# Kernel optimization log

Measured on AMD Instinct MI355X. Metric: run time of the kernel, lower is better.

The kernel has to match this reference:

```python
import jax, jax.numpy as jnp
import numpy as np

H = W = 256          # full-res feature map (2h x 2w)
WIN = 16             # window size
STRIDE = 2           # shifted-window stride
HEADS = 8
DIM_HEAD = 64
INNER = HEADS * DIM_HEAD
DIM = 128
KEEP = 50            # min(int(0.7*(256//16)**2), 50)
IOU_THR = 0.2


def _make_windows():
    xs = np.arange(0, W - WIN + 1, STRIDE)
    ys = np.arange(0, H - WIN + 1, STRIDE)
    gx, gy = np.meshgrid(xs, ys)
    return np.stack([gx.ravel(), gy.ravel(), gx.ravel() + WIN - 1, gy.ravel() + WIN - 1], axis=1)

_WIN_NP = _make_windows()          # [M,4] = (x1,y1,x2,y2), M = 121*121 = 14641
BOXES = jnp.asarray(_WIN_NP, dtype=jnp.float32)
SXY = jnp.asarray(_WIN_NP[:, :2], dtype=jnp.int32)   # integer (sx, sy) origins

# torchvision roi_align (spatial_scale=1, sampling_ratio->ceil(15/16)=1, aligned=False):
_off = (np.arange(WIN) + 0.5) * (WIN - 1.0) / WIN
LO = jnp.asarray(np.floor(_off).astype(np.int32))      # low integer index, in [0,14]
FR = jnp.asarray((_off - np.floor(_off)).astype(np.float32))


def _nms_keep(scores):
    """Greedy NMS over the fixed window grid; returns top-KEEP kept indices."""
    x1, y1, x2, y2 = BOXES[:, 0], BOXES[:, 1], BOXES[:, 2], BOXES[:, 3]
    area = (x2 - x1) * (y2 - y1)

    def body(k, carry):
        live, keep = carry
        idx = jnp.argmax(jnp.where(live, scores, -jnp.inf))
        bb = BOXES[idx]
        iw = jnp.clip(jnp.minimum(x2, bb[2]) - jnp.maximum(x1, bb[0]), 0.0)
        ih = jnp.clip(jnp.minimum(y2, bb[3]) - jnp.maximum(y1, bb[1]), 0.0)
        inter = iw * ih
        iou = inter / (area + area[idx] - inter)
        live = live & (iou <= IOU_THR)
        return live, keep.at[k].set(idx.astype(jnp.int32))

    _, keep = jax.lax.fori_loop(
        0, KEEP, body,
        (jnp.ones(BOXES.shape[0], bool), jnp.zeros(KEEP, jnp.int32)))
    return keep


def _forward(x, prob, fix_w, w_qkv, w_out, b_out):
    b = prob.shape[0]
    d = x.shape[-1]
    # entropy map at half res
    entropy = -jnp.sum(prob * jnp.log2(prob + 1e-10), axis=1)          # [b,128,128]
    # FixCNN: 8x8 ones-init conv, VALID -> [b,1,121,121]; normalized window score
    score = jax.lax.conv_general_dilated(
        entropy[:, None], fix_w, (1, 1), 'VALID',
        dimension_numbers=('NCHW', 'OIHW', 'NCHW'))
    score = score.reshape(b, -1) / float((WIN // 2) * (WIN // 2))      # [b,14641]

    keep = jax.lax.stop_gradient(jax.vmap(_nms_keep)(score))           # [b,KEEP]
    sx = SXY[keep][..., 0]                                             # [b,KEEP]
    sy = SXY[keep][..., 1]

    x2d = x.reshape(b, H, W, d)   # token n = h*W + w (channels-last layout)
    ar = jnp.arange(WIN)

    def gather_one(xi, syi, sxi):  # xi [H,W,d]
        R = syi[:, None, None] + ar[None, :, None]
        C = sxi[:, None, None] + ar[None, None, :]
        return xi[R, C]

    crops = jax.vmap(gather_one)(x2d, sy, sx)                          # [b,K,16,16,d]

    # roi_align bilinear sampling with fixed fractional grid
    c00 = crops[:, :, LO[:, None], LO[None, :]]
    c01 = crops[:, :, LO[:, None], LO[None, :] + 1]
    c10 = crops[:, :, LO[:, None] + 1, LO[None, :]]
    c11 = crops[:, :, LO[:, None] + 1, LO[None, :] + 1]
    fy = FR[:, None, None]
    fx = FR[None, :, None]
    win = ((1 - fy) * (1 - fx) * c00 + (1 - fy) * fx * c01
           + fy * (1 - fx) * c10 + fy * fx * c11)                      # [b,K,16,16,d]

    toks = win.reshape(b * KEEP, WIN * WIN, d)                         # [m,256,d]
    qkv = toks @ w_qkv.T                                               # [m,256,3*INNER]
    q, k_, v = jnp.split(qkv, 3, axis=-1)

    def to_heads(t):
        return t.reshape(t.shape[0], t.shape[1], HEADS, DIM_HEAD).transpose(0, 2, 1, 3)

    q, k_, v = to_heads(q), to_heads(k_), to_heads(v)
    attn = jax.nn.softmax(jnp.einsum('mhnd,mhkd->mhnk', q, k_) * (DIM_HEAD ** -0.5), axis=-1)
    out = jnp.einsum('mhnk,mhkd->mhnd', attn, v)
    out = out.transpose(0, 2, 1, 3).reshape(b * KEEP, WIN * WIN, INNER)
    out = out @ w_out.T + b_out                                        # [m,256,d]

    # overlap scatter-add + count normalization
    out2d = out.reshape(b, KEEP, WIN, WIN, d)
    bidx = jnp.arange(b)[:, None, None, None]
    Y = sy[:, :, None, None] + ar[None, None, :, None]
    X = sx[:, :, None, None] + ar[None, None, None, :]
    acc = jnp.zeros((b, H, W, d), x.dtype).at[bidx, Y, X].add(out2d)
    cnt = jnp.zeros((b, H, W), x.dtype).at[bidx, Y, X].add(1.0)
    outx = (acc / (cnt[..., None] + 1e-10)).reshape(b, H * W, d)
    return x + outx


def setup_inputs() -> dict:
    key = jax.random.key(0)
    ks = jax.random.split(key, 4)
    b = 4
    x = jax.random.normal(ks[0], (b, H * W, DIM), dtype=jnp.float32)
    prob = jax.random.uniform(ks[1], (b, 2, H // 2, W // 2), dtype=jnp.float32)
    fix_w = jnp.ones((1, 1, WIN // 2, WIN // 2), dtype=jnp.float32)
    w_qkv = jax.random.normal(ks[2], (3 * INNER, DIM), dtype=jnp.float32) * 0.02
    w_out = jax.random.normal(ks[3], (DIM, INNER), dtype=jnp.float32) * 0.02
    b_out = jnp.zeros((DIM,), dtype=jnp.float32)
    return {"x": x, "prob": prob, "fix_w": fix_w, "w_qkv": w_qkv, "w_out": w_out, "b_out": b_out}


def reference(x, prob, fix_w, w_qkv, w_out, b_out):
    return _forward(x, prob, fix_w, w_qkv, w_out, b_out)
```

## Files before the change

kernel.cpp:

```cpp
#include <hip/hip_runtime.h>
#include <math.h>

#define NB 4
#define NWIN 121
#define NBOX (NWIN*NWIN)
#define NKEEP 50
#define HWD 256
#define DIM 128
#define HEADS 8
#define NTOK 256
#define NWTOT (NB*NKEEP)

#define OFF_ENT   0
#define OFF_SCORE 65536
#define OFF_KEEP  124160
#define OFF_WQKV  124288
#define OFF_WOUT  222592
#define OFF_TOKBF 255360
#define OFF_PO    3532160
#define WS_FLOATS 6808960

#define KPAD 76
#define VPAD 268

typedef __attribute__((ext_vector_type(8))) short short8;
typedef __attribute__((ext_vector_type(4))) short short4v;
typedef __attribute__((ext_vector_type(4))) float f32x4;

static __device__ __forceinline__ unsigned short f2bf(float f) {
  union { float f; unsigned u; } v; v.f = f;
  unsigned r = (v.u + 0x7fffu + ((v.u >> 16) & 1u)) >> 16;
  return (unsigned short)r;
}
static __device__ __forceinline__ short4v pk4(f32x4 a) {
  short4v r;
  r[0] = (short)f2bf(a[0]); r[1] = (short)f2bf(a[1]);
  r[2] = (short)f2bf(a[2]); r[3] = (short)f2bf(a[3]);
  return r;
}
static __device__ __forceinline__ short8 ld8_lds(const unsigned short* p) {
  short4v a = *(const short4v*)p;
  short4v b = *(const short4v*)(p + 4);
  short8 r;
  r[0]=a[0]; r[1]=a[1]; r[2]=a[2]; r[3]=a[3];
  r[4]=b[0]; r[5]=b[1]; r[6]=b[2]; r[7]=b[3];
  return r;
}
static __device__ __forceinline__ short8 ld8_g(const unsigned short* p) {
  return *(const short8*)p;
}

template<int CTRL>
static __device__ __forceinline__ float dppmax(float v) {
  union { float f; int i; } a, r; a.f = v;
  r.i = __builtin_amdgcn_update_dpp(a.i, a.i, CTRL, 0xf, 0xf, false);
  return fmaxf(v, r.f);
}

__global__ void k_entropy(const float* __restrict__ prob, float* __restrict__ ent) {
  int idx = blockIdx.x * 256 + threadIdx.x;
  int b = idx >> 14, p = idx & 16383;
  float p0 = prob[(size_t)(b * 2) * 16384 + p];
  float p1 = prob[(size_t)(b * 2 + 1) * 16384 + p];
  ent[idx] = -(p0 * log2f(p0 + 1e-10f) + p1 * log2f(p1 + 1e-10f));
}

__global__ void k_score(const float* __restrict__ ent, const float* __restrict__ fw,
                        float* __restrict__ sc) {
  int gid = blockIdx.x * 256 + threadIdx.x;
  if (gid >= NB * NBOX) return;
  int b = gid / NBOX, rem = gid % NBOX;
  int oy = rem / NWIN, ox = rem % NWIN;
  const float* e = ent + b * 16384 + oy * 128 + ox;
  float s = 0.f;
#pragma unroll
  for (int r = 0; r < 8; ++r)
#pragma unroll
    for (int c = 0; c < 8; ++c)
      s += e[r * 128 + c] * fw[r * 8 + c];
  sc[gid] = s * (1.0f / 64.0f);
}

__global__ void k_nms(const float* __restrict__ scores, int* __restrict__ keep) {
  __shared__ float sc[NWIN * 128];
  int b = blockIdx.x, l = threadIdx.x;
  for (int idx = l; idx < NWIN * 128; idx += 64) {
    int r = idx >> 7, c = idx & 127;
    float v = (c < NWIN) ? scores[b * NBOX + r * NWIN + c] : -INFINITY;
    sc[(r << 7) + (c ^ ((r & 7) << 2))] = v;
  }
  float M0 = -INFINITY, M1 = -INFINITY; int C0 = 0, C1 = 0;
#pragma unroll
  for (int slot = 0; slot < 2; ++slot) {
    int r = l + slot * 64;
    if (slot == 1 && r >= NWIN) break;
    int r7 = (r & 7) << 2, rbase = r << 7;
    float bv0=-INFINITY,bv1=-INFINITY,bv2=-INFINITY,bv3=-INFINITY;
    int bc0=0,bc1=0,bc2=0,bc3=0;
    for (int lb = 0; lb < 32; ++lb) {
      f32x4 v = *(const f32x4*)&sc[rbase + ((lb << 2) ^ r7)];
      int c0 = lb << 2;
      if (v[0] > bv0) { bv0 = v[0]; bc0 = c0; }
      if (v[1] > bv1) { bv1 = v[1]; bc1 = c0 + 1; }
      if (v[2] > bv2) { bv2 = v[2]; bc2 = c0 + 2; }
      if (v[3] > bv3) { bv3 = v[3]; bc3 = c0 + 3; }
    }
    float bv = bv0; int bc = bc0;
    if (bv1 > bv || (bv1 == bv && bc1 < bc)) { bv = bv1; bc = bc1; }
    if (bv2 > bv || (bv2 == bv && bc2 < bc)) { bv = bv2; bc = bc2; }
    if (bv3 > bv || (bv3 == bv && bc3 < bc)) { bv = bv3; bc = bc3; }
    if (slot == 0) { M0 = bv; C0 = bc; } else { M1 = bv; C1 = bc; }
  }

  for (int k = 0; k < NKEEP; ++k) {
    float g = fmaxf(M0, M1);
    g = dppmax<0x111>(g); g = dppmax<0x112>(g);
    g = dppmax<0x114>(g); g = dppmax<0x118>(g);
    g = dppmax<0x142>(g); g = dppmax<0x143>(g);
    union { float f; int i; } gi, gm; gi.f = g;
    gm.i = __builtin_amdgcn_readlane(gi.i, 63);
    float gmax = gm.f;
    unsigned long long b0 = __ballot(M0 == gmax);
    unsigned long long b1 = __ballot(M1 == gmax);
    int R;
    if (b0) R = __ffsll((unsigned long long)b0) - 1;
    else    R = 64 + __ffsll((unsigned long long)b1) - 1;
    int Cc = (R < 64) ? __builtin_amdgcn_readlane(C0, R)
                      : __builtin_amdgcn_readlane(C1, R - 64);
    if (l == 0) {
      keep[(b * NKEEP + k) * 2 + 0] = 2 * R;
      keep[(b * NKEEP + k) * 2 + 1] = 2 * Cc;
    }
    bool kill0 = false, kill1 = false;
    {
      int dy = l - R, ady = dy < 0 ? -dy : dy;
      if (ady <= 4) {
        int ih = 15 - 2 * ady;
#pragma unroll
        for (int dx = -4; dx <= 4; ++dx) {
          int adx = dx < 0 ? -dx : dx;
          if ((15 - 2 * adx) * ih > 75) {
            int cc = Cc + dx;
            if ((unsigned)cc < (unsigned)NWIN)
              sc[(l << 7) + (cc ^ ((l & 7) << 2))] = -INFINITY;
          }
        }
        int adx = C0 - Cc; adx = adx < 0 ? -adx : adx;
        kill0 = (adx <= 4) && ((15 - 2 * adx) * ih > 75);
      }
    }
    if (l + 64 < NWIN) {
      int r1 = l + 64;
      int dy = r1 - R, ady = dy < 0 ? -dy : dy;
      if (ady <= 4) {
        int ih = 15 - 2 * ady;
#pragma unroll
        for (int dx = -4; dx <= 4; ++dx) {
          int adx = dx < 0 ? -dx : dx;
          if ((15 - 2 * adx) * ih > 75) {
            int cc = Cc + dx;
            if ((unsigned)cc < (unsigned)NWIN)
              sc[(r1 << 7) + (cc ^ ((r1 & 7) << 2))] = -INFINITY;
          }
        }
        int adx = C1 - Cc; adx = adx < 0 ? -adx : adx;
        kill1 = (adx <= 4) && ((15 - 2 * adx) * ih > 75);
      }
    }
    if (__any(kill0 | kill1)) {
      int r = kill0 ? l : (kill1 ? l + 64 : l);
      int r7 = (r & 7) << 2, rbase = r << 7;
      float bv0=-INFINITY,bv1=-INFINITY,bv2=-INFINITY,bv3=-INFINITY;
      int bc0=0,bc1=0,bc2=0,bc3=0;
      for (int lb = 0; lb < 32; ++lb) {
        f32x4 v = *(const f32x4*)&sc[rbase + ((lb << 2) ^ r7)];
        int c0 = lb << 2;
        if (v[0] > bv0) { bv0 = v[0]; bc0 = c0; }
        if (v[1] > bv1) { bv1 = v[1]; bc1 = c0 + 1; }
        if (v[2] > bv2) { bv2 = v[2]; bc2 = c0 + 2; }
        if (v[3] > bv3) { bv3 = v[3]; bc3 = c0 + 3; }
      }
      float bv = bv0; int bc = bc0;
      if (bv1 > bv || (bv1 == bv && bc1 < bc)) { bv = bv1; bc = bc1; }
      if (bv2 > bv || (bv2 == bv && bc2 < bc)) { bv = bv2; bc = bc2; }
      if (bv3 > bv || (bv3 == bv && bc3 < bc)) { bv = bv3; bc = bc3; }
      if (kill0) { M0 = bv; C0 = bc; }
      else if (kill1) { M1 = bv; C1 = bc; }
    }
  }
}

__global__ void k_wcvt(const float* __restrict__ wqkv, const float* __restrict__ wout,
                       unsigned short* __restrict__ wqkv_bf, unsigned short* __restrict__ wout_bf) {
  int i = blockIdx.x * 256 + threadIdx.x;
  if (i < 196608) wqkv_bf[i] = f2bf(wqkv[i]);
  int j = i - 196608;
  if (j >= 0 && j < 65536) wout_bf[j] = f2bf(wout[j]);
}

__global__ void k_toks(const float* __restrict__ x, const int* __restrict__ keep,
                       unsigned short* __restrict__ tokbf) {
  int w = blockIdx.x;
  int b = w / NKEEP;
  int sy = keep[w * 2 + 0], sx = keep[w * 2 + 1];
  int tid = threadIdx.x;
  int ch = tid & 127, th = tid >> 7;
  const float* xb = x + (size_t)b * 65536 * DIM;
  for (int it = 0; it < 128; ++it) {
    int tk = it * 2 + th;
    int i = tk >> 4, j = tk & 15;
    float offy = (i + 0.5f) * 0.9375f;
    float offx = (j + 0.5f) * 0.9375f;
    int li = (int)offy, lj = (int)offx;
    float fy = offy - (float)li, fx = offx - (float)lj;
    const float* p = xb + ((size_t)((sy + li) * HWD + (sx + lj))) * DIM + ch;
    float v00 = p[0], v01 = p[DIM], v10 = p[HWD * DIM], v11 = p[HWD * DIM + DIM];
    float w00 = (1.f - fy) * (1.f - fx), w01 = (1.f - fy) * fx;
    float w10 = fy * (1.f - fx), w11 = fy * fx;
    tokbf[((size_t)w * NTOK + tk) * DIM + ch] = f2bf(w00 * v00 + w01 * v01 + w10 * v10 + w11 * v11);
  }
}

__global__ __launch_bounds__(512, 2) void k_attn(
    const unsigned short* __restrict__ tokbf,
    const unsigned short* __restrict__ wqkv,
    const unsigned short* __restrict__ wout,
    unsigned short* __restrict__ po) {
  __shared__ __align__(16) char smem[112128];
  unsigned short* Klds = (unsigned short*)smem;
  unsigned short* VT   = (unsigned short*)(smem + 38912);
  const int tid = threadIdx.x;
  const int wv = tid >> 6, ln = tid & 63;
  const int lo = ln & 15, hi = ln >> 4;
  const int win = blockIdx.x;
  unsigned short* QP = (unsigned short*)(smem + 73216 + wv * 4864);
  const unsigned short* tw = tokbf + (size_t)win * NTOK * DIM;
  const int qrow = wv * 32;

  f32x4 pacc[8][2];
#pragma unroll
  for (int mf = 0; mf < 8; ++mf)
#pragma unroll
    for (int nf = 0; nf < 2; ++nf) pacc[mf][nf] = (f32x4){0.f,0.f,0.f,0.f};

  for (int h = 0; h < HEADS; ++h) {
    if (h) __syncthreads();

    {
      f32x4 kacc[4][2];
#pragma unroll
      for (int mf = 0; mf < 4; ++mf)
#pragma unroll
        for (int nf = 0; nf < 2; ++nf) kacc[mf][nf] = (f32x4){0.f,0.f,0.f,0.f};
#pragma unroll
      for (int kf = 0; kf < 4; ++kf) {
        short8 aw[4], bt[2];
#pragma unroll
        for (int mf = 0; mf < 4; ++mf)
          aw[mf] = ld8_g(wqkv + (size_t)(512 + h * 64 + mf * 16 + lo) * 128 + kf * 32 + hi * 8);
#pragma unroll
        for (int nf = 0; nf < 2; ++nf)
          bt[nf] = ld8_g(&tw[(qrow + nf * 16 + lo) * 128 + kf * 32 + hi * 8]);
#pragma unroll
        for (int mf = 0; mf < 4; ++mf)
#pragma unroll
          for (int nf = 0; nf < 2; ++nf)
            kacc[mf][nf] = __builtin_amdgcn_mfma_f32_16x16x32_bf16(aw[mf], bt[nf], kacc[mf][nf], 0, 0, 0);
      }
#pragma unroll
      for (int mf = 0; mf < 4; ++mf)
#pragma unroll
        for (int nf = 0; nf < 2; ++nf)
          *(short4v*)&Klds[(qrow + nf * 16 + lo) * KPAD + mf * 16 + hi * 4] = pk4(kacc[mf][nf]);
    }
    {
      f32x4 vacc[2][4];
#pragma unroll
      for (int mf = 0; mf < 2; ++mf)
#pragma unroll
        for (int nf = 0; nf < 4; ++nf) vacc[mf][nf] = (f32x4){0.f,0.f,0.f,0.f};
#pragma unroll
      for (int kf = 0; kf < 4; ++kf) {
        short8 at[2], bw[4];
#pragma unroll
        for (int mf = 0; mf < 2; ++mf)
          at[mf] = ld8_g(&tw[(qrow + mf * 16 + lo) * 128 + kf * 32 + hi * 8]);
#pragma unroll
        for (int nf = 0; nf < 4; ++nf)
          bw[nf] = ld8_g(wqkv + (size_t)(1024 + h * 64 + nf * 16 + lo) * 128 + kf * 32 + hi * 8);
#pragma unroll
        for (int mf = 0; mf < 2; ++mf)
#pragma unroll
          for (int nf = 0; nf < 4; ++nf)
            vacc[mf][nf] = __builtin_amdgcn_mfma_f32_16x16x32_bf16(at[mf], bw[nf], vacc[mf][nf], 0, 0, 0);
      }
#pragma unroll
      for (int mf = 0; mf < 2; ++mf)
#pragma unroll
        for (int nf = 0; nf < 4; ++nf)
          *(short4v*)&VT[(nf * 16 + lo) * VPAD + qrow + mf * 16 + hi * 4] = pk4(vacc[mf][nf]);
    }
    {
      f32x4 qacc[4][2];
#pragma unroll
      for (int mf = 0; mf < 4; ++mf)
#pragma unroll
        for (int nf = 0; nf < 2; ++nf) qacc[mf][nf] = (f32x4){0.f,0.f,0.f,0.f};
#pragma unroll
      for (int kf = 0; kf < 4; ++kf) {
        short8 aw[4], bt[2];
#pragma unroll
        for (int mf = 0; mf < 4; ++mf)
          aw[mf] = ld8_g(wqkv + (size_t)(h * 64 + mf * 16 + lo) * 128 + kf * 32 + hi * 8);
#pragma unroll
        for (int nf = 0; nf < 2; ++nf)
          bt[nf] = ld8_g(&tw[(qrow + nf * 16 + lo) * 128 + kf * 32 + hi * 8]);
#pragma unroll
        for (int mf = 0; mf < 4; ++mf)
#pragma unroll
          for (int nf = 0; nf < 2; ++nf)
            qacc[mf][nf] = __builtin_amdgcn_mfma_f32_16x16x32_bf16(aw[mf], bt[nf], qacc[mf][nf], 0, 0, 0);
      }
#pragma unroll
      for (int mf = 0; mf < 4; ++mf)
#pragma unroll
        for (int nf = 0; nf < 2; ++nf)
          *(short4v*)&QP[(nf * 16 + lo) * KPAD + mf * 16 + hi * 4] = pk4(qacc[mf][nf] * 0.125f);
    }
    __syncthreads();

    short8 Qb[2][2];
#pragma unroll
    for (int nf = 0; nf < 2; ++nf)
#pragma unroll
      for (int kf = 0; kf < 2; ++kf)
        Qb[nf][kf] = ld8_lds(&QP[(nf * 16 + lo) * KPAD + kf * 32 + hi * 8]);

    f32x4 Ot[4][2];
#pragma unroll
    for (int mf = 0; mf < 4; ++mf)
#pragma unroll
      for (int nf = 0; nf < 2; ++nf) Ot[mf][nf] = (f32x4){0.f,0.f,0.f,0.f};
    float mrow[2] = {-INFINITY, -INFINITY};
    float lrow[2] = {0.f, 0.f};

    for (int ck = 0; ck < 4; ++ck) {
      f32x4 sacc[4][2];
#pragma unroll
      for (int mf = 0; mf < 4; ++mf)
#pragma unroll
        for (int nf = 0; nf < 2; ++nf) sacc[mf][nf] = (f32x4){0.f,0.f,0.f,0.f};
      short8 ka[4][2];
#pragma unroll
      for (int mf = 0; mf < 4; ++mf)
#pragma unroll
        for (int kf = 0; kf < 2; ++kf)
          ka[mf][kf] = ld8_lds(&Klds[(ck * 64 + mf * 16 + lo) * KPAD + kf * 32 + hi * 8]);
#pragma unroll
      for (int mf = 0; mf < 4; ++mf)
#pragma unroll
        for (int nf = 0; nf < 2; ++nf)
#pragma unroll
          for (int kf = 0; kf < 2; ++kf)
            sacc[mf][nf] = __builtin_amdgcn_mfma_f32_16x16x32_bf16(ka[mf][kf], Qb[nf][kf], sacc[mf][nf], 0, 0, 0);

#pragma unroll
      for (int nf = 0; nf < 2; ++nf) {
        float cmax = -INFINITY;
#pragma unroll
        for (int mf = 0; mf < 4; ++mf)
#pragma unroll
          for (int r = 0; r < 4; ++r) cmax = fmaxf(cmax, sacc[mf][nf][r]);
        cmax = fmaxf(cmax, __shfl_xor(cmax, 16));
        cmax = fmaxf(cmax, __shfl_xor(cmax, 32));
        float mnew = fmaxf(mrow[nf], cmax);
        float corr = __expf(mrow[nf] - mnew);
        float ps = 0.f;
#pragma unroll
        for (int mf = 0; mf < 4; ++mf)
#pragma unroll
          for (int r = 0; r < 4; ++r) {
            float e = __expf(sacc[mf][nf][r] - mnew);
            sacc[mf][nf][r] = e; ps += e;
          }
        ps += __shfl_xor(ps, 16);
        ps += __shfl_xor(ps, 32);
        lrow[nf] = lrow[nf] * corr + ps;
        mrow[nf] = mnew;
#pragma unroll
        for (int mf = 0; mf < 4; ++mf) Ot[mf][nf] *= corr;
      }
#pragma unroll
      for (int mf = 0; mf < 4; ++mf)
#pragma unroll
        for (int nf = 0; nf < 2; ++nf)
          *(short4v*)&QP[(nf * 16 + lo) * KPAD + mf * 16 + hi * 4] = pk4(sacc[mf][nf]);
      short8 pb[2][2], va[4][2];
#pragma unroll
      for (int nf = 0; nf < 2; ++nf)
#pragma unroll
        for (int kf = 0; kf < 2; ++kf)
          pb[nf][kf] = ld8_lds(&QP[(nf * 16 + lo) * KPAD + kf * 32 + hi * 8]);
#pragma unroll
      for (int mf = 0; mf < 4; ++mf)
#pragma unroll
        for (int kf = 0; kf < 2; ++kf)
          va[mf][kf] = ld8_lds(&VT[(mf * 16 + lo) * VPAD + ck * 64 + kf * 32 + hi * 8]);
#pragma unroll
      for (int mf = 0; mf < 4; ++mf)
#pragma unroll
        for (int nf = 0; nf < 2; ++nf)
#pragma unroll
          for (int kf = 0; kf < 2; ++kf)
            Ot[mf][nf] = __builtin_amdgcn_mfma_f32_16x16x32_bf16(va[mf][kf], pb[nf][kf], Ot[mf][nf], 0, 0, 0);
    }

#pragma unroll
    for (int nf = 0; nf < 2; ++nf) {
      float inv = 1.f / lrow[nf];
#pragma unroll
      for (int mf = 0; mf < 4; ++mf)
        *(short4v*)&QP[(nf * 16 + lo) * KPAD + mf * 16 + hi * 4] = pk4(Ot[mf][nf] * inv);
    }
    short8 Ob[2][2];
#pragma unroll
    for (int nf = 0; nf < 2; ++nf)
#pragma unroll
      for (int kf = 0; kf < 2; ++kf)
        Ob[nf][kf] = ld8_lds(&QP[(nf * 16 + lo) * KPAD + kf * 32 + hi * 8]);
#pragma unroll
    for (int kf = 0; kf < 2; ++kf) {
      short8 aw[8];
#pragma unroll
      for (int mf = 0; mf < 8; ++mf)
        aw[mf] = ld8_g(wout + (size_t)(mf * 16 + lo) * 512 + h * 64 + kf * 32 + hi * 8);
#pragma unroll
      for (int mf = 0; mf < 8; ++mf)
#pragma unroll
        for (int nf = 0; nf < 2; ++nf)
          pacc[mf][nf] = __builtin_amdgcn_mfma_f32_16x16x32_bf16(aw[mf], Ob[nf][kf], pacc[mf][nf], 0, 0, 0);
    }
  }

#pragma unroll
  for (int mf = 0; mf < 8; ++mf)
#pragma unroll
    for (int nf = 0; nf < 2; ++nf)
      *(short4v*)&po[((size_t)win * NTOK + qrow + nf * 16 + lo) * 128 + mf * 16 + hi * 4] = pk4(pacc[mf][nf]);
}

__global__ void k_final(const float* __restrict__ x, const unsigned short* __restrict__ po,
                        const int* __restrict__ keep, const float* __restrict__ bout,
                        float* __restrict__ out) {
  __shared__ int kp[2 * NKEEP];
  int tid = threadIdx.x;
  int gid = blockIdx.x * 256 + tid;
  int chq = gid & 3, pix = gid >> 2;
  int b = pix >> 16, pb = pix & 65535, y = pb >> 8, xx = pb & 255;
  if (tid < 2 * NKEEP) kp[tid] = keep[b * 2 * NKEEP + tid];
  __syncthreads();
  float acc[32];
#pragma unroll
  for (int i = 0; i < 32; ++i) acc[i] = 0.f;
  float cnt = 0.f;
  for (int w = 0; w < NKEEP; ++w) {
    int dy = y - kp[2 * w], dx = xx - kp[2 * w + 1];
    if ((unsigned)dy < 16u && (unsigned)dx < 16u) {
      cnt += 1.f;
      const unsigned short* pp = po + ((size_t)(b * NKEEP + w) * NTOK + dy * 16 + dx) * 128 + chq * 32;
#pragma unroll
      for (int k2 = 0; k2 < 4; ++k2) {
        short8 v = ld8_g(pp + k2 * 8);
#pragma unroll
        for (int j = 0; j < 8; ++j) {
          union { unsigned u; float f; } cv;
          cv.u = ((unsigned)(unsigned short)v[j]) << 16;
          acc[k2 * 8 + j] += cv.f;
        }
      }
    }
  }
  size_t base = (size_t)pix * 128 + chq * 32;
  float inv = 1.f / (cnt + 1e-10f);
#pragma unroll
  for (int i = 0; i < 32; ++i)
    out[base + i] = x[base + i] + (acc[i] + cnt * bout[chq * 32 + i]) * inv;
}

extern "C" void kernel_launch(void* const* d_in, const int* in_sizes, int n_in,
                              void* d_out, int out_size, void* d_ws, size_t ws_size,
                              hipStream_t stream) {
  const float* x    = (const float*)d_in[0];
  const float* prob = (const float*)d_in[1];
  const float* fixw = (const float*)d_in[2];
  const float* wqkv = (const float*)d_in[3];
  const float* wout = (const float*)d_in[4];
  const float* bout = (const float*)d_in[5];
  float* out = (float*)d_out;
  float* ws  = (float*)d_ws;
  if (ws_size < WS_FLOATS * sizeof(float)) return;

  float* ent  = ws + OFF_ENT;
  float* sc   = ws + OFF_SCORE;
  int*   keep = (int*)(ws + OFF_KEEP);
  unsigned short* wqkv_bf = (unsigned short*)(ws + OFF_WQKV);
  unsigned short* wout_bf = (unsigned short*)(ws + OFF_WOUT);
  unsigned short* tokbf   = (unsigned short*)(ws + OFF_TOKBF);
  unsigned short* po      = (unsigned short*)(ws + OFF_PO);

  k_entropy<<<256, 256, 0, stream>>>(prob, ent);
  k_score<<<(NB * NBOX + 255) / 256, 256, 0, stream>>>(ent, fixw, sc);
  k_wcvt<<<1024, 256, 0, stream>>>(wqkv, wout, wqkv_bf, wout_bf);
  k_nms<<<NB, 64, 0, stream>>>(sc, keep);
  k_toks<<<NWTOT, 256, 0, stream>>>(x, keep, tokbf);
  k_attn<<<NWTOT, 512, 0, stream>>>(tokbf, wqkv_bf, wout_bf, po);
  k_final<<<NB * 65536 * 4 / 256, 256, 0, stream>>>(x, po, keep, bout, out);
}
```

Measured before the change: 486.7 us.

## Pre-swizzle padded score layout and recompute killed NMS rows wave-cooperatively

The score kernel now writes scores directly into the padded, XOR-swizzled 121x128 layout NMS uses, with -inf padding. This lets the single-wave NMS block load its shared copy with plain vector copies instead of scalar gathers and index remapping. Rows whose maximum was suppressed are now rescanned one at a time by the whole wave, using a DPP reduction and ballot, instead of each affected lane scanning its whole row serially. The cost is a serial loop over killed rows, each needing a wave reduction, plus a slightly larger workspace.

```diff
diff --git a/kernel.cpp b/kernel.cpp
--- a/kernel.cpp
+++ b/kernel.cpp
@@ -10,15 +10,16 @@
 #define HEADS 8
 #define NTOK 256
 #define NWTOT (NB*NKEEP)
+#define SCPAD 15616
 
 #define OFF_ENT   0
 #define OFF_SCORE 65536
-#define OFF_KEEP  124160
-#define OFF_WQKV  124288
-#define OFF_WOUT  222592
-#define OFF_TOKBF 255360
-#define OFF_PO    3532160
-#define WS_FLOATS 6808960
+#define OFF_KEEP  128128
+#define OFF_WQKV  128256
+#define OFF_WOUT  226560
+#define OFF_TOKBF 259328
+#define OFF_PO    3536128
+#define WS_FLOATS 6812928
 
 #define KPAD 76
 #define VPAD 268
@@ -56,6 +57,14 @@
   r.i = __builtin_amdgcn_update_dpp(a.i, a.i, CTRL, 0xf, 0xf, false);
   return fmaxf(v, r.f);
 }
+static __device__ __forceinline__ float wavemax(float v) {
+  v = dppmax<0x111>(v); v = dppmax<0x112>(v);
+  v = dppmax<0x114>(v); v = dppmax<0x118>(v);
+  v = dppmax<0x142>(v); v = dppmax<0x143>(v);
+  union { float f; int i; } gi, gm; gi.f = v;
+  gm.i = __builtin_amdgcn_readlane(gi.i, 63);
+  return gm.f;
+}
 
 __global__ void k_entropy(const float* __restrict__ prob, float* __restrict__ ent) {
   int idx = blockIdx.x * 256 + threadIdx.x;
@@ -66,28 +75,41 @@
 }
 
 __global__ void k_score(const float* __restrict__ ent, const float* __restrict__ fw,
-                        float* __restrict__ sc) {
+                        float* __restrict__ scp) {
   int gid = blockIdx.x * 256 + threadIdx.x;
-  if (gid >= NB * NBOX) return;
-  int b = gid / NBOX, rem = gid % NBOX;
-  int oy = rem / NWIN, ox = rem % NWIN;
-  const float* e = ent + b * 16384 + oy * 128 + ox;
-  float s = 0.f;
-#pragma unroll
-  for (int r = 0; r < 8; ++r)
-#pragma unroll
-    for (int c = 0; c < 8; ++c)
-      s += e[r * 128 + c] * fw[r * 8 + c];
-  sc[gid] = s * (1.0f / 64.0f);
-}
-
-__global__ void k_nms(const float* __restrict__ scores, int* __restrict__ keep) {
-  __shared__ float sc[NWIN * 128];
+  if (gid >= NB * SCPAD) return;
+  int b = gid / SCPAD, idx = gid % SCPAD;
+  int r = idx >> 7, c = idx & 127;
+  float s = -INFINITY;
+  if (r < NWIN && c < NWIN) {
+    const float* e = ent + b * 16384 + r * 128 + c;
+    float a = 0.f;
+#pragma unroll
+    for (int rr = 0; rr < 8; ++rr)
+#pragma unroll
+      for (int cc = 0; cc < 8; ++cc)
+        a += e[rr * 128 + cc] * fw[rr * 8 + cc];
+    s = a * (1.0f / 64.0f);
+  }
+  scp[b * SCPAD + (r << 7) + (c ^ ((r & 7) << 2))] = s;
+}
+
+__global__ void k_nms(const float* __restrict__ scp, int* __restrict__ keep) {
+  __shared__ float sc[SCPAD];
   int b = blockIdx.x, l = threadIdx.x;
-  for (int idx = l; idx < NWIN * 128; idx += 64) {
-    int r = idx >> 7, c = idx & 127;
-    float v = (c < NWIN) ? scores[b * NBOX + r * NWIN + c] : -INFINITY;
-    sc[(r << 7) + (c ^ ((r & 7) << 2))] = v;
+  const float* src = scp + b * SCPAD;
+  for (int cb = 0; cb < 64; cb += 8) {
+    f32x4 t[8];
+#pragma unroll
+    for (int i = 0; i < 8; ++i) {
+      int idx = (cb + i) * 256 + l * 4;
+      if (idx < SCPAD) t[i] = *(const f32x4*)&src[idx];
+    }
+#pragma unroll
+    for (int i = 0; i < 8; ++i) {
+      int idx = (cb + i) * 256 + l * 4;
+      if (idx < SCPAD) *(f32x4*)&sc[idx] = t[i];
+    }
   }
   float M0 = -INFINITY, M1 = -INFINITY; int C0 = 0, C1 = 0;
 #pragma unroll
@@ -113,13 +135,7 @@
   }
 
   for (int k = 0; k < NKEEP; ++k) {
-    float g = fmaxf(M0, M1);
-    g = dppmax<0x111>(g); g = dppmax<0x112>(g);
-    g = dppmax<0x114>(g); g = dppmax<0x118>(g);
-    g = dppmax<0x142>(g); g = dppmax<0x143>(g);
-    union { float f; int i; } gi, gm; gi.f = g;
-    gm.i = __builtin_amdgcn_readlane(gi.i, 63);
-    float gmax = gm.f;
+    float gmax = wavemax(fmaxf(M0, M1));
     unsigned long long b0 = __ballot(M0 == gmax);
     unsigned long long b1 = __ballot(M1 == gmax);
     int R;
@@ -167,25 +183,25 @@
         kill1 = (adx <= 4) && ((15 - 2 * adx) * ih > 75);
       }
     }
-    if (__any(kill0 | kill1)) {
-      int r = kill0 ? l : (kill1 ? l + 64 : l);
-      int r7 = (r & 7) << 2, rbase = r << 7;
-      float bv0=-INFINITY,bv1=-INFINITY,bv2=-INFINITY,bv3=-INFINITY;
-      int bc0=0,bc1=0,bc2=0,bc3=0;
-      for (int lb = 0; lb < 32; ++lb) {
-        f32x4 v = *(const f32x4*)&sc[rbase + ((lb << 2) ^ r7)];
-        int c0 = lb << 2;
-        if (v[0] > bv0) { bv0 = v[0]; bc0 = c0; }
-        if (v[1] > bv1) { bv1 = v[1]; bc1 = c0 + 1; }
-        if (v[2] > bv2) { bv2 = v[2]; bc2 = c0 + 2; }
-        if (v[3] > bv3) { bv3 = v[3]; bc3 = c0 + 3; }
-      }
-      float bv = bv0; int bc = bc0;
-      if (bv1 > bv || (bv1 == bv && bc1 < bc)) { bv = bv1; bc = bc1; }
-      if (bv2 > bv || (bv2 == bv && bc2 < bc)) { bv = bv2; bc = bc2; }
-      if (bv3 > bv || (bv3 == bv && bc3 < bc)) { bv = bv3; bc = bc3; }
-      if (kill0) { M0 = bv; C0 = bc; }
-      else if (kill1) { M1 = bv; C1 = bc; }
+    unsigned long long need0 = __ballot(kill0);
+    unsigned long long need1 = __ballot(kill1);
+    while (need0 | need1) {
+      int rr;
+      if (need0) { rr = __ffsll((unsigned long long)need0) - 1; need0 &= need0 - 1; }
+      else       { rr = __ffsll((unsigned long long)need1) - 1 + 64; need1 &= need1 - 1; }
+      int r7 = (rr & 7) << 2, rbase = rr << 7;
+      float v0 = sc[rbase + (l ^ r7)];
+      float v1 = sc[rbase + ((l + 64) ^ r7)];
+      float rmax = wavemax(fmaxf(v0, v1));
+      unsigned long long e0 = __ballot(v0 == rmax);
+      unsigned long long e1 = __ballot(v1 == rmax);
+      int bc;
+      if (e0) bc = __ffsll((unsigned long long)e0) - 1;
+      else    bc = 64 + __ffsll((unsigned long long)e1) - 1;
+      if (l == (rr & 63)) {
+        if (rr >= 64) { M1 = rmax; C1 = bc; }
+        else          { M0 = rmax; C0 = bc; }
+      }
     }
   }
 }
@@ -501,7 +517,7 @@
   if (ws_size < WS_FLOATS * sizeof(float)) return;
 
   float* ent  = ws + OFF_ENT;
-  float* sc   = ws + OFF_SCORE;
+  float* scp  = ws + OFF_SCORE;
   int*   keep = (int*)(ws + OFF_KEEP);
   unsigned short* wqkv_bf = (unsigned short*)(ws + OFF_WQKV);
   unsigned short* wout_bf = (unsigned short*)(ws + OFF_WOUT);
@@ -509,9 +525,9 @@
   unsigned short* po      = (unsigned short*)(ws + OFF_PO);
 
   k_entropy<<<256, 256, 0, stream>>>(prob, ent);
-  k_score<<<(NB * NBOX + 255) / 256, 256, 0, stream>>>(ent, fixw, sc);
+  k_score<<<(NB * SCPAD + 255) / 256, 256, 0, stream>>>(ent, fixw, scp);
   k_wcvt<<<1024, 256, 0, stream>>>(wqkv, wout, wqkv_bf, wout_bf);
-  k_nms<<<NB, 64, 0, stream>>>(sc, keep);
+  k_nms<<<NB, 64, 0, stream>>>(scp, keep);
   k_toks<<<NWTOT, 256, 0, stream>>>(x, keep, tokbf);
   k_attn<<<NWTOT, 512, 0, stream>>>(tokbf, wqkv_bf, wout_bf, po);
   k_final<<<NB * 65536 * 4 / 256, 256, 0, stream>>>(x, po, keep, bout, out);
```

Result: faster. 390.2 us (-19.8%).
